# Kernel tuning notes

Hardware: AMD Instinct MI355X
Metric: run time of the kernel (lower is better)

The kernel has to match this reference:

```python
import jax, jax.numpy as jnp
import numpy as np
from jax import lax

B, CIN, COUT, K = 4, 128, 128, 3
Z = X = Y = 32
EPS = 1e-8


def setup_inputs() -> dict:
    key = jax.random.key(0)
    k1, k2, k3 = jax.random.split(key, 3)
    x = jax.random.normal(k1, (B, CIN, Z, X, Y), dtype=jnp.float32)
    S = jax.random.normal(k2, (B, CIN), dtype=jnp.float32)
    weight = jax.random.normal(k3, (COUT, CIN, K, K, K), dtype=jnp.float32)
    return {"x": x, "S": S, "weight": weight}


def reference(x, S, weight):
    b, cin, z, xx, yy = x.shape
    cout = weight.shape[0]
    # Per-sample modulated weight: [B, cout, cin, k, k, k]
    W = weight[None] * (S[:, None, :, None, None, None] + 1.0)
    # Demodulation: L2-normalize each (b, cout) filter
    d = lax.rsqrt(jnp.sum(W * W, axis=(2, 3, 4, 5), keepdims=True) + EPS)
    W = W * d
    # Grouped conv3d with groups=B (stride=1, dilation=1 -> same padding = (k-1)//2)
    pad = (K - 1) // 2
    xr = x.reshape(1, b * cin, z, xx, yy)
    Wr = W.reshape(b * cout, cin, K, K, K)
    out = lax.conv_general_dilated(
        xr, Wr,
        window_strides=(1, 1, 1),
        padding=[(pad, pad)] * 3,
        feature_group_count=b,
        dimension_numbers=("NCDHW", "OIDHW", "NCDHW"),
    )
    return out.reshape(b, cout, z, xx, yy)
```

## Files before the change

### kernel.cpp

```cpp
#include <hip/hip_runtime.h>

#define B_    4
#define CIN_  128
#define COUT_ 128
#define EPSF  1e-8f

typedef short  short8  __attribute__((ext_vector_type(8)));
typedef unsigned short ushort8 __attribute__((ext_vector_type(8)));
typedef float  f32x16  __attribute__((ext_vector_type(16)));

__device__ __forceinline__ unsigned short f2bf(float f) {
    union { float f; unsigned int u; } v; v.f = f;
    unsigned int r = (v.u + 0x7fffu + ((v.u >> 16) & 1u)) >> 16;
    return (unsigned short)r;
}

__global__ __launch_bounds__(256) void wt_scale_kernel(const float* __restrict__ w,
                                                       const float* __restrict__ S,
                                                       unsigned short* __restrict__ wtf,
                                                       float* __restrict__ dscale) {
    __shared__ float red[128];
    const int bx = blockIdx.x;
    const int tid = threadIdx.x;
    if (bx < 1728) {
        int idx = bx * 256 + tid;
        int e  = idx & 7;
        int l  = (idx >> 3) & 63;
        int c  = (idx >> 9) & 7;
        int ct = (idx >> 12) & 3;
        int ko = idx >> 14;
        int co = ct * 32 + (l & 31);
        int ci = c * 16 + (l >> 5) * 8 + e;
        wtf[idx] = f2bf(w[((size_t)co * CIN_ + ci) * 27 + ko]);
    } else {
        const int co = bx - 1728;
        const int ci = tid & 127;
        const float* wp = w + ((size_t)co * CIN_ + ci) * 27;
        float wsq = 0.f;
#pragma unroll
        for (int k = 0; k < 27; ++k) { float v = wp[k]; wsq += v * v; }
        for (int b = 0; b < B_; ++b) {
            float s = S[b * CIN_ + ci] + 1.0f;
            red[ci] = s * s * wsq;
            __syncthreads();
            for (int off = 64; off > 0; off >>= 1) {
                if (tid < off) red[tid] += red[tid + off];
                __syncthreads();
            }
            if (tid == 0) dscale[b * COUT_ + co] = rsqrtf(red[0] + EPSF);
            __syncthreads();
        }
    }
}

__global__ __launch_bounds__(256) void xt_kernel(const float* __restrict__ x,
                                                 const float* __restrict__ S,
                                                 unsigned short* __restrict__ xT) {
    __shared__ float ls[128 * 33];
    const int xx = blockIdx.x, z = blockIdx.y, b = blockIdx.z;
    const int tid = threadIdx.x;
    const size_t base = (size_t)b * 4194304 + (size_t)z * 1024 + xx * 32;
#pragma unroll
    for (int it = 0; it < 4; ++it) {
        int i = tid + it * 256;
        int ci = i >> 3, y4 = (i & 7) * 4;
        float4 v = *(const float4*)(x + base + (size_t)ci * 32768 + y4);
        float s = S[b * CIN_ + ci] + 1.0f;
        ls[ci * 33 + y4 + 0] = v.x * s;
        ls[ci * 33 + y4 + 1] = v.y * s;
        ls[ci * 33 + y4 + 2] = v.z * s;
        ls[ci * 33 + y4 + 3] = v.w * s;
    }
    __syncthreads();
    const size_t obase = (size_t)((b * 32 + z) * 32 + xx) * 4096;
#pragma unroll
    for (int it = 0; it < 2; ++it) {
        int i = tid + it * 256;
        int y = i >> 4, c = (i >> 1) & 7, h = i & 1;
        ushort8 v;
#pragma unroll
        for (int j = 0; j < 8; ++j) v[j] = f2bf(ls[(c * 16 + h * 8 + j) * 33 + y]);
        *(ushort8*)(xT + obase + c * 512 + y * 16 + h * 8) = v;
    }
}

__global__ __launch_bounds__(256, 2) void conv_mfma(const unsigned short* __restrict__ xT,
                                                    const unsigned short* __restrict__ wtf,
                                                    const float* __restrict__ dscale,
                                                    float* __restrict__ out) {
    __shared__ char smem[2][26112];
    const int tid  = threadIdx.x;
    const int lane = tid & 63;
    const int wv   = tid >> 6;
    const int z0 = (blockIdx.x >> 4) * 4;
    const int x0 = (blockIdx.x & 15) * 2;
    const int b  = blockIdx.y;

    int goff[7];
    const int lbase = tid * 16;
#pragma unroll
    for (int s = 0; s < 7; ++s) {
        int g = tid + s * 256;
        goff[s] = -2;
        if (g < 1632) {
            int row = g / 68, rem = g - row * 68;
            int h = rem / 34, yi = rem - h * 34;
            int zg = z0 + (row >> 2) - 1;
            int xg = x0 + (row & 3) - 1;
            goff[s] = -1;
            if ((unsigned)zg < 32u && (unsigned)xg < 32u && yi >= 1 && yi <= 32)
                goff[s] = ((b * 32 + zg) * 32 + xg) * 8192 + (yi - 1) * 32 + h * 16;
        }
    }

    const char* xTb = (const char*)xT;
    const char* wtb = (const char*)wtf;
    const int bperlane = ((lane >> 5) * 34 + (lane & 31)) * 16;
    const int aperlane = lane * 16;

    f32x16 acc[4][2];
#pragma unroll
    for (int cz = 0; cz < 4; ++cz)
#pragma unroll
        for (int cx = 0; cx < 2; ++cx)
#pragma unroll
            for (int r = 0; r < 16; ++r) acc[cz][cx][r] = 0.f;

    ushort8 st[7];
#pragma unroll
    for (int s = 0; s < 7; ++s) {
        ushort8 v = {0, 0, 0, 0, 0, 0, 0, 0};
        if (goff[s] >= 0) v = *(const ushort8*)(xTb + goff[s]);
        st[s] = v;
    }
#pragma unroll
    for (int s = 0; s < 7; ++s)
        if (goff[s] != -2) *(ushort8*)(&smem[0][0] + lbase + s * 4096) = st[s];
    __syncthreads();

    for (int c = 0; c < 8; ++c) {
        if (c < 7) {
#pragma unroll
            for (int s = 0; s < 7; ++s) {
                ushort8 v = {0, 0, 0, 0, 0, 0, 0, 0};
                if (goff[s] >= 0) v = *(const ushort8*)(xTb + goff[s] + (c + 1) * 1024);
                st[s] = v;
            }
        }
        const char* buf   = smem[c & 1];
        const char* abase = wtb + c * 1024 + wv * 8192;
#pragma unroll
        for (int ky = 0; ky < 3; ++ky) {
            short8 a[9];
#pragma unroll
            for (int t = 0; t < 9; ++t)
                a[t] = *(const short8*)(abase + (t * 3 + ky) * 32768 + aperlane);
#pragma unroll
            for (int zr = 0; zr < 6; ++zr) {
                short8 bf[4];
#pragma unroll
                for (int xr = 0; xr < 4; ++xr)
                    bf[xr] = *(const short8*)(buf + ((zr * 4 + xr) * 68 + ky) * 16 + bperlane);
#pragma unroll
                for (int cz = 0; cz < 4; ++cz) {
                    const int kz = zr - cz;
                    if (kz >= 0 && kz <= 2) {
#pragma unroll
                        for (int cx = 0; cx < 2; ++cx)
#pragma unroll
                        for (int kx = 0; kx < 3; ++kx)
                            acc[cz][cx] = __builtin_amdgcn_mfma_f32_32x32x16_bf16(
                                a[kz * 3 + kx], bf[cx + kx], acc[cz][cx], 0, 0, 0);
                    }
                }
            }
        }
        if (c < 7) {
            char* nbuf = (char*)smem[(c + 1) & 1];
#pragma unroll
            for (int s = 0; s < 7; ++s)
                if (goff[s] != -2) *(ushort8*)(nbuf + lbase + s * 4096) = st[s];
        }
        __syncthreads();
    }

    float dd[16];
#pragma unroll
    for (int r = 0; r < 16; ++r)
        dd[r] = dscale[b * COUT_ + wv * 32 + (r & 3) + 8 * (r >> 2) + 4 * (lane >> 5)];
#pragma unroll
    for (int cz = 0; cz < 4; ++cz)
#pragma unroll
    for (int cx = 0; cx < 2; ++cx) {
        size_t ob = (((size_t)(b * COUT_ + wv * 32) * 32 + (z0 + cz)) * 32 + (x0 + cx)) * 32 + (lane & 31);
#pragma unroll
        for (int r = 0; r < 16; ++r) {
            int row = (r & 3) + 8 * (r >> 2) + 4 * (lane >> 5);
            out[ob + (size_t)row * 32768] = acc[cz][cx][r] * dd[r];
        }
    }
}

__global__ __launch_bounds__(256, 4) void conv_kernel(const float* __restrict__ x,
                                                      const float* __restrict__ S,
                                                      const float* __restrict__ w,
                                                      const float* __restrict__ dscale,
                                                      float* __restrict__ out) {
    __shared__ float xs[6][6][36];
    __shared__ float wsm[27][16];
    const int tid = threadIdx.x;
    const int zt  = blockIdx.x >> 3;
    const int xt  = blockIdx.x & 7;
    const int co0 = blockIdx.y * 16;
    const int b   = blockIdx.z;
    const int z0 = zt * 4, x0 = xt * 4;
    const int lane = tid & 63;
    const int cg = tid >> 6;
    const int zz = (lane >> 4) & 3;
    const int xx = (lane >> 2) & 3;
    const int y0 = (lane & 3) * 8;
    float acc[4][8];
#pragma unroll
    for (int c = 0; c < 4; ++c)
#pragma unroll
        for (int j = 0; j < 8; ++j) acc[c][j] = 0.f;
    for (int ci = 0; ci < CIN_; ++ci) {
        __syncthreads();
        const float* xb = x + (size_t)(b * CIN_ + ci) * 32768;
        const float smod = S[b * CIN_ + ci] + 1.0f;
#pragma unroll
        for (int t = 0; t < 5; ++t) {
            int i = tid + t * 256;
            if (i < 6 * 6 * 34) {
                int zi = i / 204, r = i - zi * 204, xi = r / 34, yi = r - xi * 34;
                int z = z0 + zi - 1, xc = x0 + xi - 1, y = yi - 1;
                float v = 0.f;
                if ((unsigned)z < 32u && (unsigned)xc < 32u && (unsigned)y < 32u)
                    v = xb[z * 1024 + xc * 32 + y] * smod;
                xs[zi][xi][yi] = v;
            }
        }
#pragma unroll
        for (int t = 0; t < 2; ++t) {
            int i = tid + t * 256;
            if (i < 16 * 27) {
                int cog2 = i / 27, k = i - cog2 * 27;
                wsm[k][cog2] = w[((size_t)(co0 + cog2) * CIN_ + ci) * 27 + k];
            }
        }
        __syncthreads();
#pragma unroll
        for (int kz = 0; kz < 3; ++kz)
#pragma unroll
        for (int kx = 0; kx < 3; ++kx) {
            const float* xrow = &xs[zz + kz][xx + kx][y0];
            float xw[10];
#pragma unroll
            for (int q = 0; q < 10; ++q) xw[q] = xrow[q];
            const int kb = (kz * 3 + kx) * 3;
#pragma unroll
            for (int ky = 0; ky < 3; ++ky) {
                float4 wvv = *(const float4*)&wsm[kb + ky][cg * 4];
#pragma unroll
                for (int j = 0; j < 8; ++j) {
                    acc[0][j] = fmaf(xw[ky + j], wvv.x, acc[0][j]);
                    acc[1][j] = fmaf(xw[ky + j], wvv.y, acc[1][j]);
                    acc[2][j] = fmaf(xw[ky + j], wvv.z, acc[2][j]);
                    acc[3][j] = fmaf(xw[ky + j], wvv.w, acc[3][j]);
                }
            }
        }
    }
#pragma unroll
    for (int c = 0; c < 4; ++c) {
        const int co = co0 + cg * 4 + c;
        const float dd = dscale[b * COUT_ + co];
        float* ob = out + (((size_t)(b * COUT_ + co) * 32 + (z0 + zz)) * 32 + (x0 + xx)) * 32 + y0;
#pragma unroll
        for (int j = 0; j < 8; ++j) ob[j] = acc[c][j] * dd;
    }
}

extern "C" void kernel_launch(void* const* d_in, const int* in_sizes, int n_in,
                              void* d_out, int out_size, void* d_ws, size_t ws_size,
                              hipStream_t stream) {
    const float* x = (const float*)d_in[0];
    const float* S = (const float*)d_in[1];
    const float* w = (const float*)d_in[2];
    float* out = (float*)d_out;

    const size_t NEED = 1048576 + 33554432;
    if (ws_size >= NEED) {
        float* dscale = (float*)d_ws;
        unsigned short* wtf = (unsigned short*)((char*)d_ws + 4096);
        unsigned short* xT  = (unsigned short*)((char*)d_ws + 1048576);
        wt_scale_kernel<<<dim3(1728 + 128), dim3(256), 0, stream>>>(w, S, wtf, dscale);
        xt_kernel<<<dim3(32, 32, 4), dim3(256), 0, stream>>>(x, S, xT);
        conv_mfma<<<dim3(128, 4), dim3(256), 0, stream>>>(xT, wtf, dscale, out);
    } else {
        float* dscale = (float*)d_ws;
        wt_scale_kernel<<<dim3(1856), dim3(256), 0, stream>>>(w, S, (unsigned short*)((char*)d_ws + 4096), dscale);
        conv_kernel<<<dim3(64, 8, 4), dim3(256), 0, stream>>>(x, S, w, dscale, out);
    }
}
```

Measured before the change: 114.0 us.

## Enlarge conv tile to 4x4 with 8 waves sharing halo and weight loads

```diff
diff --git a/kernel.cpp b/kernel.cpp
--- a/kernel.cpp
+++ b/kernel.cpp
@@ -84,29 +84,62 @@
     }
 }
 
-__global__ __launch_bounds__(256, 2) void conv_mfma(const unsigned short* __restrict__ xT,
+template<int KY>
+__device__ __forceinline__ void section(const char* buf, const char* abase,
+                                        int aperlane, int bperlane, int xh2,
+                                        f32x16 (&acc)[4][2]) {
+    short8 a[9];
+#pragma unroll
+    for (int t = 0; t < 9; ++t)
+        a[t] = *(const short8*)(abase + (t * 3 + KY) * 32768 + aperlane);
+#pragma unroll
+    for (int zr = 0; zr < 6; ++zr) {
+        short8 bf[4];
+#pragma unroll
+        for (int xr = 0; xr < 4; ++xr)
+            bf[xr] = *(const short8*)(buf + ((zr * 6 + xh2 + xr) * 68 + KY) * 16 + bperlane);
+        __builtin_amdgcn_s_setprio(1);
+#pragma unroll
+        for (int cz = 0; cz < 4; ++cz) {
+            const int kz = zr - cz;
+            if (kz >= 0 && kz <= 2) {
+#pragma unroll
+                for (int cx = 0; cx < 2; ++cx)
+#pragma unroll
+                for (int kx = 0; kx < 3; ++kx)
+                    acc[cz][cx] = __builtin_amdgcn_mfma_f32_32x32x16_bf16(
+                        a[kz * 3 + kx], bf[cx + kx], acc[cz][cx], 0, 0, 0);
+            }
+        }
+        __builtin_amdgcn_s_setprio(0);
+    }
+}
+
+__global__ __launch_bounds__(512, 1) void conv_mfma(const unsigned short* __restrict__ xT,
                                                     const unsigned short* __restrict__ wtf,
                                                     const float* __restrict__ dscale,
                                                     float* __restrict__ out) {
-    __shared__ char smem[2][26112];
+    __shared__ char smem[2][39168];
     const int tid  = threadIdx.x;
     const int lane = tid & 63;
     const int wv   = tid >> 6;
-    const int z0 = (blockIdx.x >> 4) * 4;
-    const int x0 = (blockIdx.x & 15) * 2;
+    const int cog  = wv & 3;
+    const int xh2  = (wv >> 2) * 2;
+    const int z0 = (blockIdx.x >> 3) * 4;
+    const int x0 = (blockIdx.x & 7) * 4;
     const int b  = blockIdx.y;
 
-    int goff[7];
+    int goff[5];
     const int lbase = tid * 16;
 #pragma unroll
-    for (int s = 0; s < 7; ++s) {
-        int g = tid + s * 256;
+    for (int s = 0; s < 5; ++s) {
+        int g = tid + s * 512;
         goff[s] = -2;
-        if (g < 1632) {
+        if (g < 2448) {
             int row = g / 68, rem = g - row * 68;
             int h = rem / 34, yi = rem - h * 34;
-            int zg = z0 + (row >> 2) - 1;
-            int xg = x0 + (row & 3) - 1;
+            int zi = row / 6, xi = row - zi * 6;
+            int zg = z0 + zi - 1, xg = x0 + xi - 1;
             goff[s] = -1;
             if ((unsigned)zg < 32u && (unsigned)xg < 32u && yi >= 1 && yi <= 32)
                 goff[s] = ((b * 32 + zg) * 32 + xg) * 8192 + (yi - 1) * 32 + h * 16;
@@ -126,60 +159,45 @@
 #pragma unroll
             for (int r = 0; r < 16; ++r) acc[cz][cx][r] = 0.f;
 
-    ushort8 st[7];
-#pragma unroll
-    for (int s = 0; s < 7; ++s) {
+    ushort8 st[5];
+#pragma unroll
+    for (int s = 0; s < 5; ++s) {
         ushort8 v = {0, 0, 0, 0, 0, 0, 0, 0};
         if (goff[s] >= 0) v = *(const ushort8*)(xTb + goff[s]);
         st[s] = v;
     }
 #pragma unroll
-    for (int s = 0; s < 7; ++s)
-        if (goff[s] != -2) *(ushort8*)(&smem[0][0] + lbase + s * 4096) = st[s];
+    for (int s = 0; s < 5; ++s)
+        if (goff[s] != -2) *(ushort8*)(&smem[0][0] + lbase + s * 8192) = st[s];
     __syncthreads();
 
     for (int c = 0; c < 8; ++c) {
         if (c < 7) {
 #pragma unroll
-            for (int s = 0; s < 7; ++s) {
+            for (int s = 0; s < 5; ++s) {
                 ushort8 v = {0, 0, 0, 0, 0, 0, 0, 0};
                 if (goff[s] >= 0) v = *(const ushort8*)(xTb + goff[s] + (c + 1) * 1024);
                 st[s] = v;
             }
         }
         const char* buf   = smem[c & 1];
-        const char* abase = wtb + c * 1024 + wv * 8192;
-#pragma unroll
-        for (int ky = 0; ky < 3; ++ky) {
-            short8 a[9];
-#pragma unroll
-            for (int t = 0; t < 9; ++t)
-                a[t] = *(const short8*)(abase + (t * 3 + ky) * 32768 + aperlane);
-#pragma unroll
-            for (int zr = 0; zr < 6; ++zr) {
-                short8 bf[4];
-#pragma unroll
-                for (int xr = 0; xr < 4; ++xr)
-                    bf[xr] = *(const short8*)(buf + ((zr * 4 + xr) * 68 + ky) * 16 + bperlane);
-#pragma unroll
-                for (int cz = 0; cz < 4; ++cz) {
-                    const int kz = zr - cz;
-                    if (kz >= 0 && kz <= 2) {
-#pragma unroll
-                        for (int cx = 0; cx < 2; ++cx)
-#pragma unroll
-                        for (int kx = 0; kx < 3; ++kx)
-                            acc[cz][cx] = __builtin_amdgcn_mfma_f32_32x32x16_bf16(
-                                a[kz * 3 + kx], bf[cx + kx], acc[cz][cx], 0, 0, 0);
-                    }
-                }
-            }
-        }
+        const char* abase = wtb + c * 1024 + cog * 8192;
+
+        if (xh2 == 0) {
+            section<0>(buf, abase, aperlane, bperlane, xh2, acc);
+            section<1>(buf, abase, aperlane, bperlane, xh2, acc);
+            section<2>(buf, abase, aperlane, bperlane, xh2, acc);
+        } else {
+            section<2>(buf, abase, aperlane, bperlane, xh2, acc);
+            section<1>(buf, abase, aperlane, bperlane, xh2, acc);
+            section<0>(buf, abase, aperlane, bperlane, xh2, acc);
+        }
+
         if (c < 7) {
             char* nbuf = (char*)smem[(c + 1) & 1];
 #pragma unroll
-            for (int s = 0; s < 7; ++s)
-                if (goff[s] != -2) *(ushort8*)(nbuf + lbase + s * 4096) = st[s];
+            for (int s = 0; s < 5; ++s)
+                if (goff[s] != -2) *(ushort8*)(nbuf + lbase + s * 8192) = st[s];
         }
         __syncthreads();
     }
@@ -187,12 +205,12 @@
     float dd[16];
 #pragma unroll
     for (int r = 0; r < 16; ++r)
-        dd[r] = dscale[b * COUT_ + wv * 32 + (r & 3) + 8 * (r >> 2) + 4 * (lane >> 5)];
+        dd[r] = dscale[b * COUT_ + cog * 32 + (r & 3) + 8 * (r >> 2) + 4 * (lane >> 5)];
 #pragma unroll
     for (int cz = 0; cz < 4; ++cz)
 #pragma unroll
     for (int cx = 0; cx < 2; ++cx) {
-        size_t ob = (((size_t)(b * COUT_ + wv * 32) * 32 + (z0 + cz)) * 32 + (x0 + cx)) * 32 + (lane & 31);
+        size_t ob = (((size_t)(b * COUT_ + cog * 32) * 32 + (z0 + cz)) * 32 + (x0 + xh2 + cx)) * 32 + (lane & 31);
 #pragma unroll
         for (int r = 0; r < 16; ++r) {
             int row = (r & 3) + 8 * (r >> 2) + 4 * (lane >> 5);
@@ -296,7 +314,7 @@
         unsigned short* xT  = (unsigned short*)((char*)d_ws + 1048576);
         wt_scale_kernel<<<dim3(1728 + 128), dim3(256), 0, stream>>>(w, S, wtf, dscale);
         xt_kernel<<<dim3(32, 32, 4), dim3(256), 0, stream>>>(x, S, xT);
-        conv_mfma<<<dim3(128, 4), dim3(256), 0, stream>>>(xT, wtf, dscale, out);
+        conv_mfma<<<dim3(64, 4), dim3(512), 0, stream>>>(xT, wtf, dscale, out);
     } else {
         float* dscale = (float*)d_ws;
         wt_scale_kernel<<<dim3(1856), dim3(256), 0, stream>>>(w, S, (unsigned short*)((char*)d_ws + 4096), dscale);
```

Result: no change. 116.2 us (+1.9%).
